# Performance work log

Measured on AMD Instinct MI355X. Metric: run time of the kernel, lower is better.

## Reference

```python
import jax, jax.numpy as jnp
import numpy as np

NUM_CLASSES = 2
IGNORE_INDEX = 0
B, H, W = 4, 512, 512
BIG_I = 2 ** 30  # int sentinel for 'no seed yet'
INF = jnp.float32(1e9)  # distance when a column/image has no seed


def _edt_to_seed(seed):
    """Exact 2D Euclidean distance transform: distance from every pixel to the
    nearest True pixel in `seed` [H, W] (matches scipy distance_transform_edt
    applied to an image whose zeros are `seed`).
    Pass 1: 1D nearest-seed distance down each column via cummax/cummin scans.
    Pass 2: exact lower envelope across rows by brute-force min over k:
            D^2(i,j) = min_k ( (j-k)^2 + g(i,k)^2 ).
    """
    h, w = seed.shape
    rows = jnp.arange(h, dtype=jnp.int32)[:, None]              # [H,1]
    last = jax.lax.cummax(jnp.where(seed, rows, -1), axis=0)     # last seed above
    d_fwd = jnp.where(last >= 0, rows - last, BIG_I)
    nxt = jax.lax.cummin(jnp.where(seed, rows, BIG_I), axis=0, reverse=True)
    d_bwd = jnp.where(nxt < BIG_I, nxt - rows, BIG_I)
    g = jnp.minimum(d_fwd, d_bwd)                                # [H,W] int
    g2 = jnp.where(g >= BIG_I // 2, INF * INF, (g * g).astype(jnp.float32))
    cols = jnp.arange(w, dtype=jnp.float32)
    sq = (cols[:, None] - cols[None, :]) ** 2                    # [Wj,Wk]
    d2 = jnp.min(g2[:, None, :] + sq[None, :, :], axis=-1)       # [H,Wj]
    return jnp.sqrt(d2)


def _distance_map_one(tgt):
    """tgt: [H, W] int labels -> [num_classes, H, W] signed distance maps."""
    maps = []
    for c in range(NUM_CLASSES):
        if c == IGNORE_INDEX:
            maps.append(jnp.zeros(tgt.shape, jnp.float32))
            continue
        mask = tgt == c
        pos_dist = _edt_to_seed(~mask)   # edt(posmask): dist to nearest background
        neg_dist = _edt_to_seed(mask)    # edt(negmask): dist to nearest foreground
        present = jnp.any(mask)          # 'if mask.sum() > 0' guard
        maps.append(jnp.where(present, neg_dist - pos_dist, 0.0))
    return jnp.stack(maps, axis=0)


def setup_inputs() -> dict:
    key = jax.random.key(0)
    k1, k2 = jax.random.split(key)
    pred = jax.random.normal(k1, (B, NUM_CLASSES, H, W), dtype=jnp.float32)
    target = jax.random.randint(k2, (B, H, W), 0, 2, dtype=jnp.int32)
    return {"pred": pred, "target": target}


def reference(pred, target):
    p = jax.nn.softmax(pred, axis=1)                         # [B,C,H,W]
    # sequential over batch to bound the [H,W,W] EDT intermediate
    dmaps = jax.lax.map(_distance_map_one, target)           # [B,C,H,W]
    return jnp.mean(p * dmaps)
```

## Files before the change

kernel.cpp:

```cpp
#include <hip/hip_runtime.h>
#include <math.h>

#define BB 4
#define HH 512
#define WW 512
#define HWSZ (HH * WW)

#define TCOLS 16
#define TCH   16
#define CROWS 32


__global__ __launch_bounds__(256) void edt_cols_kernel(
    const int* __restrict__ target,
    unsigned int* __restrict__ gpack,
    int* __restrict__ counts)
{
    int blk = blockIdx.x;
    int b = blk >> 5;
    int tile = blk & 31;
    int tid = threadIdx.x;
    int c = tid & (TCOLS - 1);
    int ch = tid >> 4;
    int j = tile * TCOLS + c;
    int r0 = ch * CROWS;

    const int* t = target + b * HWSZ + j;

    unsigned int maskN = 0;
#pragma unroll
    for (int i = 0; i < CROWS; ++i)
        maskN |= (unsigned int)(t[(r0 + i) * WW] == 1) << i;
    unsigned int maskP = ~maskN;

    __shared__ short sLastN[TCH][TCOLS], sLastP[TCH][TCOLS];
    __shared__ short sFirstN[TCH][TCOLS], sFirstP[TCH][TCOLS];
    __shared__ short sBefN[TCH][TCOLS], sBefP[TCH][TCOLS];
    __shared__ short sAftN[TCH][TCOLS], sAftP[TCH][TCOLS];
    __shared__ int sCnt;

    sLastN[ch][c]  = maskN ? (short)(r0 + 31 - __builtin_clz(maskN)) : (short)-1;
    sFirstN[ch][c] = maskN ? (short)(r0 + __builtin_ctz(maskN))      : (short)-1;
    sLastP[ch][c]  = maskP ? (short)(r0 + 31 - __builtin_clz(maskP)) : (short)-1;
    sFirstP[ch][c] = maskP ? (short)(r0 + __builtin_ctz(maskP))      : (short)-1;
    if (tid == 0) sCnt = 0;
    __syncthreads();

    if (tid < TCOLS) {
        short befN = -1, befP = -1;
        for (int k = 0; k < TCH; ++k) {
            sBefN[k][tid] = befN; sBefP[k][tid] = befP;
            short ln = sLastN[k][tid], lp = sLastP[k][tid];
            if (ln >= 0) befN = ln;
            if (lp >= 0) befP = lp;
        }
        short aftN = -1, aftP = -1;
        for (int k = TCH - 1; k >= 0; --k) {
            sAftN[k][tid] = aftN; sAftP[k][tid] = aftP;
            short fn = sFirstN[k][tid], fp = sFirstP[k][tid];
            if (fn >= 0) aftN = fn;
            if (fp >= 0) aftP = fp;
        }
    }
    atomicAdd(&sCnt, __popc(maskN));
    __syncthreads();

    int befN = sBefN[ch][c], befP = sBefP[ch][c];
    int aftN = sAftN[ch][c], aftP = sAftP[ch][c];
    unsigned int* gp = gpack + b * HWSZ + j;

#pragma unroll
    for (int i = 0; i < CROWS; ++i) {
        int row = r0 + i;
        unsigned int belowN = maskN << (31 - i);
        unsigned int aboveN = maskN >> i;
        unsigned int dfN = belowN ? (unsigned int)__builtin_clz(belowN)
                                  : (befN >= 0 ? (unsigned int)(row - befN) : 0xFFFFu);
        unsigned int dbN = aboveN ? (unsigned int)__builtin_ctz(aboveN)
                                  : (aftN >= 0 ? (unsigned int)(aftN - row) : 0xFFFFu);
        unsigned int gN = dfN < dbN ? dfN : dbN;

        unsigned int belowP = maskP << (31 - i);
        unsigned int aboveP = maskP >> i;
        unsigned int dfP = belowP ? (unsigned int)__builtin_clz(belowP)
                                  : (befP >= 0 ? (unsigned int)(row - befP) : 0xFFFFu);
        unsigned int dbP = aboveP ? (unsigned int)__builtin_ctz(aboveP)
                                  : (aftP >= 0 ? (unsigned int)(aftP - row) : 0xFFFFu);
        unsigned int gP = dfP < dbP ? dfP : dbP;

        gp[row * WW] = gN | (gP << 16);
    }

    if (tid == 0) counts[blk] = sCnt;
}

__global__ __launch_bounds__(256) void edt_rows_kernel(
    const unsigned int* __restrict__ gpack,
    const float* __restrict__ pred,
    double* __restrict__ partials)
{
    __shared__ float g2n[WW];
    __shared__ float g2p[WW];
    __shared__ double red[256];

    int bi = blockIdx.x;
    int b = bi >> 9;
    int i = bi & (HH - 1);
    int tid = threadIdx.x;

    const unsigned int* gp = gpack + b * HWSZ + i * WW;
    for (int k = tid; k < WW; k += 256) {
        unsigned int pk = gp[k];
        unsigned int gN = pk & 0xFFFFu;
        unsigned int gP = pk >> 16;
        g2n[k] = (gN == 0xFFFFu) ? 1e18f : (float)(gN * gN);
        g2p[k] = (gP == 0xFFFFu) ? 1e18f : (float)(gP * gP);
    }
    __syncthreads();

    const float* p0 = pred + (b * 2 + 0) * HWSZ + i * WW;
    const float* p1 = pred + (b * 2 + 1) * HWSZ + i * WW;

    double local = 0.0;
    for (int j = tid; j < WW; j += 256) {
        float bn = g2n[j];
        float bp = g2p[j];
        for (int r = 1; r < WW; ++r) {
            float sq = (float)(r * r);
            if (sq >= bn && sq >= bp) break;
            int kl = j - r;
            int kr = j + r;
            if (kl >= 0) {
                bn = fminf(bn, sq + g2n[kl]);
                bp = fminf(bp, sq + g2p[kl]);
            }
            if (kr < WW) {
                bn = fminf(bn, sq + g2n[kr]);
                bp = fminf(bp, sq + g2p[kr]);
            }
        }
        float dist = sqrtf(bn) - sqrtf(bp);
        float prob = 1.0f / (1.0f + expf(p0[j] - p1[j]));
        local += (double)(prob * dist);
    }

    red[tid] = local;
    __syncthreads();
    for (int off = 128; off > 0; off >>= 1) {
        if (tid < off) red[tid] += red[tid + off];
        __syncthreads();
    }
    if (tid == 0) partials[bi] = red[0];
}

__global__ __launch_bounds__(256) void finalize_kernel(
    const int* __restrict__ counts,
    const double* __restrict__ partials,
    float* __restrict__ out)
{
    __shared__ int sPres[BB];
    __shared__ double red[256];
    int tid = threadIdx.x;

    if (tid < BB) sPres[tid] = 0;
    __syncthreads();
    if (tid < 128) atomicAdd(&sPres[tid >> 5], counts[tid]);
    __syncthreads();

    double s = 0.0;
    for (int idx = tid; idx < BB * HH; idx += 256) {
        double g = (sPres[idx >> 9] > 0) ? 1.0 : 0.0;
        s += partials[idx] * g;
    }
    red[tid] = s;
    __syncthreads();
    for (int off = 128; off > 0; off >>= 1) {
        if (tid < off) red[tid] += red[tid + off];
        __syncthreads();
    }
    if (tid == 0)
        out[0] = (float)(red[0] * (1.0 / 2097152.0));
}

extern "C" void kernel_launch(void* const* d_in, const int* in_sizes, int n_in,
                              void* d_out, int out_size, void* d_ws, size_t ws_size,
                              hipStream_t stream) {
    const float* pred = (const float*)d_in[0];
    const int* target = (const int*)d_in[1];
    float* out = (float*)d_out;

    char* ws = (char*)d_ws;
    int* counts = (int*)(ws + 0);
    double* partials = (double*)(ws + 1024);
    unsigned int* gpack = (unsigned int*)(ws + 32768);

    edt_cols_kernel<<<BB * (WW / TCOLS), 256, 0, stream>>>(target, gpack, counts);
    edt_rows_kernel<<<BB * HH, 256, 0, stream>>>(gpack, pred, partials);
    finalize_kernel<<<1, 256, 0, stream>>>(counts, partials, out);
}
```

Before: 76.02 us.

## Fuse finalize into rows kernel via last-block ticket; retile column pass

Removes the separate finalize launch: each row block reduces with wavefront shuffles, atomically adds its partial into one of 32 double slots, and the last block (found by a ticket counter) applies the per-batch presence guard and writes the output. The column kernel now uses 8-column by 16-row chunks, giving twice as many blocks, and zeroes the slots and ticket. It also switches to the fast __expf and float accumulation inside each thread. Dropping one launch and the tree reduction trades for atomic contention and a small loss of accumulation precision.

```diff
diff --git a/kernel.cpp b/kernel.cpp
--- a/kernel.cpp
+++ b/kernel.cpp
@@ -6,24 +6,34 @@
 #define WW 512
 #define HWSZ (HH * WW)
 
-#define TCOLS 16
-#define TCH   16
-#define CROWS 32
+#define TCOLS 8
+#define TCH   32
+#define CROWS 16
+#define NBLK_COLS (BB * (WW / TCOLS))
+#define NBLK_ROWS (BB * HH)
+#define NSLOTS 32
 
 
 __global__ __launch_bounds__(256) void edt_cols_kernel(
     const int* __restrict__ target,
     unsigned int* __restrict__ gpack,
-    int* __restrict__ counts)
+    int* __restrict__ counts,
+    double* __restrict__ slots,
+    int* __restrict__ ticket)
 {
     int blk = blockIdx.x;
-    int b = blk >> 5;
-    int tile = blk & 31;
+    int b = blk >> 6;
+    int tile = blk & 63;
     int tid = threadIdx.x;
     int c = tid & (TCOLS - 1);
-    int ch = tid >> 4;
+    int ch = tid >> 3;
     int j = tile * TCOLS + c;
     int r0 = ch * CROWS;
+
+    if (blk == 0) {
+        if (tid < NSLOTS) slots[tid] = 0.0;
+        if (tid == NSLOTS) *ticket = 0;
+    }
 
     const int* t = target + b * HWSZ + j;
 
@@ -31,7 +41,7 @@
 #pragma unroll
     for (int i = 0; i < CROWS; ++i)
         maskN |= (unsigned int)(t[(r0 + i) * WW] == 1) << i;
-    unsigned int maskP = ~maskN;
+    unsigned int maskP = maskN ^ 0xFFFFu;
 
     __shared__ short sLastN[TCH][TCOLS], sLastP[TCH][TCOLS];
     __shared__ short sFirstN[TCH][TCOLS], sFirstP[TCH][TCOLS];
@@ -97,11 +107,17 @@
 __global__ __launch_bounds__(256) void edt_rows_kernel(
     const unsigned int* __restrict__ gpack,
     const float* __restrict__ pred,
-    double* __restrict__ partials)
+    const int* __restrict__ counts,
+    double* __restrict__ slots,
+    int* __restrict__ ticket,
+    float* __restrict__ out)
 {
     __shared__ float g2n[WW];
     __shared__ float g2p[WW];
-    __shared__ double red[256];
+    __shared__ double wred[4];
+    __shared__ int isLast;
+    __shared__ int sPres[BB];
+    __shared__ double sSum[NSLOTS];
 
     int bi = blockIdx.x;
     int b = bi >> 9;
@@ -116,12 +132,13 @@
         g2n[k] = (gN == 0xFFFFu) ? 1e18f : (float)(gN * gN);
         g2p[k] = (gP == 0xFFFFu) ? 1e18f : (float)(gP * gP);
     }
+    if (tid < BB) sPres[tid] = 0;
     __syncthreads();
 
     const float* p0 = pred + (b * 2 + 0) * HWSZ + i * WW;
     const float* p1 = pred + (b * 2 + 1) * HWSZ + i * WW;
 
-    double local = 0.0;
+    float local = 0.0f;
     for (int j = tid; j < WW; j += 256) {
         float bn = g2n[j];
         float bp = g2p[j];
@@ -140,46 +157,39 @@
             }
         }
         float dist = sqrtf(bn) - sqrtf(bp);
-        float prob = 1.0f / (1.0f + expf(p0[j] - p1[j]));
-        local += (double)(prob * dist);
-    }
-
-    red[tid] = local;
-    __syncthreads();
-    for (int off = 128; off > 0; off >>= 1) {
-        if (tid < off) red[tid] += red[tid + off];
+        float prob = 1.0f / (1.0f + __expf(p0[j] - p1[j]));
+        local += prob * dist;
+    }
+
+#pragma unroll
+    for (int off = 32; off > 0; off >>= 1)
+        local += __shfl_down(local, off, 64);
+    if ((tid & 63) == 0) wred[tid >> 6] = (double)local;
+    __syncthreads();
+
+    if (tid == 0) {
+        double partial = wred[0] + wred[1] + wred[2] + wred[3];
+        atomicAdd(&slots[b * 8 + (bi & 7)], partial);
+        __threadfence();
+        int old = atomicAdd(ticket, 1);
+        isLast = (old == NBLK_ROWS - 1);
+    }
+    __syncthreads();
+
+    if (isLast) {
+        if (counts[tid] > 0) atomicOr(&sPres[tid >> 6], 1);
+        if (tid < NSLOTS) sSum[tid] = atomicAdd(&slots[tid], 0.0);
         __syncthreads();
-    }
-    if (tid == 0) partials[bi] = red[0];
-}
-
-__global__ __launch_bounds__(256) void finalize_kernel(
-    const int* __restrict__ counts,
-    const double* __restrict__ partials,
-    float* __restrict__ out)
-{
-    __shared__ int sPres[BB];
-    __shared__ double red[256];
-    int tid = threadIdx.x;
-
-    if (tid < BB) sPres[tid] = 0;
-    __syncthreads();
-    if (tid < 128) atomicAdd(&sPres[tid >> 5], counts[tid]);
-    __syncthreads();
-
-    double s = 0.0;
-    for (int idx = tid; idx < BB * HH; idx += 256) {
-        double g = (sPres[idx >> 9] > 0) ? 1.0 : 0.0;
-        s += partials[idx] * g;
-    }
-    red[tid] = s;
-    __syncthreads();
-    for (int off = 128; off > 0; off >>= 1) {
-        if (tid < off) red[tid] += red[tid + off];
-        __syncthreads();
-    }
-    if (tid == 0)
-        out[0] = (float)(red[0] * (1.0 / 2097152.0));
+        if (tid == 0) {
+            double tot = 0.0;
+            for (int bb = 0; bb < BB; ++bb) {
+                double s = 0.0;
+                for (int k = 0; k < 8; ++k) s += sSum[bb * 8 + k];
+                if (sPres[bb]) tot += s;
+            }
+            out[0] = (float)(tot * (1.0 / 2097152.0));
+        }
+    }
 }
 
 extern "C" void kernel_launch(void* const* d_in, const int* in_sizes, int n_in,
@@ -191,10 +201,10 @@
 
     char* ws = (char*)d_ws;
     int* counts = (int*)(ws + 0);
-    double* partials = (double*)(ws + 1024);
+    double* slots = (double*)(ws + 1024);
+    int* ticket = (int*)(ws + 1536);
     unsigned int* gpack = (unsigned int*)(ws + 32768);
 
-    edt_cols_kernel<<<BB * (WW / TCOLS), 256, 0, stream>>>(target, gpack, counts);
-    edt_rows_kernel<<<BB * HH, 256, 0, stream>>>(gpack, pred, partials);
-    finalize_kernel<<<1, 256, 0, stream>>>(counts, partials, out);
+    edt_cols_kernel<<<NBLK_COLS, 256, 0, stream>>>(target, gpack, counts, slots, ticket);
+    edt_rows_kernel<<<NBLK_ROWS, 256, 0, stream>>>(gpack, pred, counts, slots, ticket, out);
 }
```

Result: slower. 112.7 us (+48.2%).
